# Kernel tuning notes

Measured on AMD Instinct MI355X. Metric: run time of the kernel, lower is better.

The kernel has to match this reference:

```python
import jax, jax.numpy as jnp
import numpy as np

DIM, HEADS, WIN = 256, 8, 8
HD = DIM // HEADS
SCALE = HD ** -0.5


def _rel_index(w):
    # Swin-style relative position index, computed statically in numpy
    coords = np.stack(np.meshgrid(np.arange(w), np.arange(w), indexing='ij'))  # (2,w,w)
    cf = coords.reshape(2, -1)                      # (2, w*w)
    rel = (cf[:, :, None] - cf[:, None, :]).transpose(1, 2, 0)  # (w*w, w*w, 2)
    rel = rel.copy()
    rel[:, :, 0] += w - 1
    rel[:, :, 1] += w - 1
    rel[:, :, 0] *= 2 * w - 1
    return rel.sum(-1)                              # (w*w, w*w)

REL_IDX = _rel_index(WIN)


def setup_inputs() -> dict:
    key = jax.random.key(0)
    ks = jax.random.split(key, 6)
    B, C, D, H, W = 8, DIM, 100, WIN, WIN
    return {
        'x': jax.random.normal(ks[0], (B, C, D, H, W), jnp.float32),
        'dwconv_w': jax.random.normal(ks[1], (C, C, 1, 3, 3), jnp.float32) * 0.02,
        'dwconv_b': jnp.zeros((C,), jnp.float32),
        'qkv_w': jax.random.normal(ks[2], (3 * C, C), jnp.float32) * 0.02,
        'qkv_b': jnp.zeros((3 * C,), jnp.float32),
        'proj_w': jax.random.normal(ks[3], (C, C), jnp.float32) * 0.02,
        'proj_b': jnp.zeros((C,), jnp.float32),
        'rpb_table': jax.random.normal(ks[4], ((2 * WIN - 1) ** 2, HEADS), jnp.float32) * 0.02,
    }


def reference(x, dwconv_w, dwconv_b, qkv_w, qkv_b, proj_w, proj_b, rpb_table):
    B, C, D, H, W = x.shape
    N = H * W
    # 'dwconv': full Conv3d, kernel (1,3,3), padding (0,1,1)
    xl = jax.lax.conv_general_dilated(
        x, dwconv_w, window_strides=(1, 1, 1),
        padding=[(0, 0), (1, 1), (1, 1)],
        dimension_numbers=('NCDHW', 'OIDHW', 'NCDHW'),
    ) + dwconv_b[None, :, None, None, None]
    # qkv: 1x1x1 conv == pointwise linear over channels
    qkv = jnp.einsum('oc,bcdhw->bodhw', qkv_w, xl) + qkv_b[None, :, None, None, None]
    # channel dim layout: (three, head, head_dim)
    qkv = qkv.reshape(B, 3, HEADS, HD, D, N)
    q, k, v = qkv[:, 0], qkv[:, 1], qkv[:, 2]      # each (B, HEADS, HD, D, N)
    attn = jnp.einsum('bhcdn,bhcdm->bdhnm', q * SCALE, k)  # (B, D, HEADS, N, N)
    bias = rpb_table[REL_IDX.reshape(-1)].reshape(N, N, HEADS).transpose(2, 0, 1)
    attn = jax.nn.softmax(attn + bias[None, None], axis=-1)
    xa = jnp.einsum('bdhnm,bhcdm->bhcdn', attn, v)  # (B, HEADS, HD, D, N)
    xa = xa.reshape(B, C, D, H, W)                  # channel = (head, head_dim)
    out = jnp.einsum('oc,bcdhw->bodhw', proj_w, xa) + proj_b[None, :, None, None, None]
    return out
```

## Files before the change

kernel.cpp:

```cpp
#include <hip/hip_runtime.h>
#include <cstdint>
#include <cstddef>

#define SCALEQ 0.17677669529663689f

typedef _Float16 half_t;
typedef _Float16 half8   __attribute__((ext_vector_type(8)));
typedef _Float16 half4v  __attribute__((ext_vector_type(4)));
typedef float    float4v __attribute__((ext_vector_type(4)));

#define WAIT_LDS()                                                            \
  do {                                                                        \
    asm volatile("s_waitcnt lgkmcnt(0)" ::: "memory");                        \
    __builtin_amdgcn_sched_barrier(0);                                        \
  } while (0)

__global__ __launch_bounds__(256) void prep_w(
    const float* __restrict__ dwconv_w, const float* __restrict__ qkv_w,
    const float* __restrict__ proj_w, const float* __restrict__ rpb,
    half_t* __restrict__ Wt, half_t* __restrict__ qw16,
    half_t* __restrict__ pw16, float* __restrict__ btab) {
  const int blk = blockIdx.x, t = threadIdx.x;
  if (blk < 144) {
    const int base = blk * 4096;
#pragma unroll
    for (int i = 0; i < 16; ++i) {
      int idx = base + i * 256 + t;
      int tap = idx >> 16;
      int og = (idx >> 12) & 15, kh = (idx >> 9) & 7;
      int l15o = (idx >> 5) & 15, c5 = idx & 31;
      int o = og * 16 + l15o, c = kh * 32 + c5;
      Wt[idx] = (half_t)dwconv_w[(o * 256 + c) * 9 + tap];
    }
  } else if (blk < 240) {
    const int base = (blk - 144) * 2048;
#pragma unroll
    for (int i = 0; i < 8; ++i) {
      int idx = base + i * 256 + t;
      float v = qkv_w[idx];
      if (idx < 65536) v *= SCALEQ;
      qw16[idx] = (half_t)v;
    }
  } else if (blk < 272) {
    const int base = (blk - 240) * 2048;
#pragma unroll
    for (int i = 0; i < 8; ++i) {
      int idx = base + i * 256 + t;
      pw16[idx] = (half_t)proj_w[idx];
    }
  } else {
    const int base = (blk - 272) * 2048;
#pragma unroll
    for (int i = 0; i < 8; ++i) {
      int idx = base + i * 256 + t;
      int hd = idx >> 12, n = (idx >> 6) & 63, m = idx & 63;
      int h1 = n >> 3, w1 = n & 7, h2 = m >> 3, w2 = m & 7;
      int ridx = (h1 - h2 + 7) * 15 + (w1 - w2 + 7);
      btab[idx] = rpb[ridx * 8 + hd];
    }
  }
}

__global__ __launch_bounds__(512)
__attribute__((amdgpu_waves_per_eu(4, 4))) void fused_all(
    const float* __restrict__ xg, const half_t* __restrict__ Wt,
    const float* __restrict__ convb, const half_t* __restrict__ qw,
    const float* __restrict__ qkvb, const float* __restrict__ btab,
    const half_t* __restrict__ pw, const float* __restrict__ projb,
    float* __restrict__ out32) {
  __shared__ __align__(16) half_t LS[36864];
  const int bd = blockIdx.x;
  const int tid = threadIdx.x;
  const int wave = tid >> 6, lane = tid & 63;
  const int l15 = lane & 15, quad = lane >> 4;
  const int head = wave;
  const int b = bd / 100, d = bd % 100;

  half_t* xlp = LS;
  half_t* xa = LS;
  float* T = (float*)LS;
  half_t* xpl = LS + 16384;
  half_t* buf = LS + 16384 + wave * 2560;
  float* tile = (float*)LS;

  const half_t* Wq0 = qw + head * 32 * 256;
  const half_t* Wk0 = qw + 65536 + head * 32 * 256;
  const half_t* Wv0 = qw + 131072 + head * 32 * 256;

  {
    const float* xb0 = xg + ((size_t)(b * 256) * 100 + d) * 64;
#pragma unroll
    for (int i = 0; i < 32; ++i) {
      const int c = i * 8 + wave;
      tile[c * 66 + lane] = xb0[(size_t)c * 6400 + lane];
    }
  }
  __syncthreads();

  half8 xr[4];
#pragma unroll
  for (int i = 0; i < 4; ++i) {
    const int c8 = wave * 4 + i;
#pragma unroll
    for (int j = 0; j < 8; ++j)
      xr[i][j] = (half_t)tile[(c8 * 8 + j) * 66 + lane];
  }
  __syncthreads();

  {
#pragma unroll
    for (int i = 0; i < 4; ++i) {
      const int c8 = wave * 4 + i;
      *(half8*)&xpl[lane * 256 + ((c8 ^ (lane & 7)) * 8)] = xr[i];
    }
    if (tid < 32) {
      half8 z = {};
      *(half8*)(xpl + 64 * 256 + tid * 8) = z;
    }
  }
  __syncthreads();

  {
    const int wwl = l15 & 7, hb = l15 >> 3;
    float4v acc[2][4];
#pragma unroll
    for (int mi = 0; mi < 2; ++mi)
#pragma unroll
      for (int ni = 0; ni < 4; ++ni) {
        float4v z = {0.f, 0.f, 0.f, 0.f};
        acc[mi][ni] = z;
      }
    const half_t* wv0 = Wt + (wave * 2) * 4096 + l15 * 32 + quad * 8;
#pragma unroll 1
    for (int tap = 0; tap < 9; ++tap) {
      const int th = tap / 3, tw = tap - th * 3;
      const half_t* wt = wv0 + tap * 65536;
      const int ww = wwl + tw;
      const int okw = (ww >= 1) & (ww <= 8);
      int rowv[4];
#pragma unroll
      for (int ni = 0; ni < 4; ++ni) {
        const int hh = hb + th + ni * 2;
        const int ok = okw & (hh >= 1) & (hh <= 8);
        rowv[ni] = ok ? ((hh - 1) * 8 + (ww - 1)) : 64;
      }
#pragma unroll
      for (int kh = 0; kh < 8; ++kh) {
        half8 af0 = *(const half8*)(wt + kh * 512);
        half8 af1 = *(const half8*)(wt + 4096 + kh * 512);
        half8 bf[4];
#pragma unroll
        for (int ni = 0; ni < 4; ++ni) {
          const int r = rowv[ni];
          bf[ni] = *(const half8*)&xpl[r * 256 + (((kh * 4 + quad) ^ (r & 7)) * 8)];
        }
#pragma unroll
        for (int ni = 0; ni < 4; ++ni) {
          acc[0][ni] = __builtin_amdgcn_mfma_f32_16x16x32_f16(af0, bf[ni], acc[0][ni], 0, 0, 0);
          acc[1][ni] = __builtin_amdgcn_mfma_f32_16x16x32_f16(af1, bf[ni], acc[1][ni], 0, 0, 0);
        }
      }
    }
#pragma unroll
    for (int mi = 0; mi < 2; ++mi) {
      const int o4 = wave * 32 + mi * 16 + quad * 4;
      const float4v b4 = *(const float4v*)&convb[o4];
      const int chunk = o4 >> 3;
      const int sub = (quad & 1) * 4;
#pragma unroll
      for (int ni = 0; ni < 4; ++ni) {
        const int px = ni * 16 + l15;
        half4v h;
        h.x = (half_t)(acc[mi][ni].x + b4.x);
        h.y = (half_t)(acc[mi][ni].y + b4.y);
        h.z = (half_t)(acc[mi][ni].z + b4.z);
        h.w = (half_t)(acc[mi][ni].w + b4.w);
        *(half4v*)&xlp[px * 256 + ((chunk ^ (px & 7)) * 8) + sub] = h;
      }
    }
  }

  __syncthreads();

  half8 aq[4];
  {
    float4v acc[2][4];
#pragma unroll
    for (int mi = 0; mi < 2; ++mi)
#pragma unroll
      for (int ni = 0; ni < 4; ++ni) {
        float4v z = {0.f, 0.f, 0.f, 0.f};
        acc[mi][ni] = z;
      }
#pragma unroll
    for (int kh = 0; kh < 8; ++kh) {
      half8 w0 = *(const half8*)(Wq0 + l15 * 256 + kh * 32 + quad * 8);
      half8 w1 = *(const half8*)(Wq0 + (16 + l15) * 256 + kh * 32 + quad * 8);
      half8 bf[4];
#pragma unroll
      for (int ni = 0; ni < 4; ++ni) {
        int r = ni * 16 + l15;
        bf[ni] = *(const half8*)&xlp[r * 256 + (((kh * 4 + quad) ^ (r & 7)) * 8)];
      }
#pragma unroll
      for (int ni = 0; ni < 4; ++ni) {
        acc[0][ni] = __builtin_amdgcn_mfma_f32_16x16x32_f16(w0, bf[ni], acc[0][ni], 0, 0, 0);
        acc[1][ni] = __builtin_amdgcn_mfma_f32_16x16x32_f16(w1, bf[ni], acc[1][ni], 0, 0, 0);
      }
    }
#pragma unroll
    for (int mi = 0; mi < 2; ++mi) {
      const float4v b4 = *(const float4v*)&qkvb[head * 32 + mi * 16 + quad * 4];
#pragma unroll
      for (int ni = 0; ni < 4; ++ni) {
        half4v h;
        h.x = (half_t)(acc[mi][ni].x + b4.x * SCALEQ);
        h.y = (half_t)(acc[mi][ni].y + b4.y * SCALEQ);
        h.z = (half_t)(acc[mi][ni].z + b4.z * SCALEQ);
        h.w = (half_t)(acc[mi][ni].w + b4.w * SCALEQ);
        *(half4v*)(buf + (ni * 16 + l15) * 40 + mi * 16 + quad * 4) = h;
      }
    }
    WAIT_LDS();
#pragma unroll
    for (int i = 0; i < 4; ++i)
      aq[i] = *(const half8*)(buf + (i * 16 + l15) * 40 + quad * 8);
    WAIT_LDS();
  }

  half8 bk[4];
  {
    float4v acc[2][4];
#pragma unroll
    for (int mi = 0; mi < 2; ++mi)
#pragma unroll
      for (int ni = 0; ni < 4; ++ni) {
        float4v z = {0.f, 0.f, 0.f, 0.f};
        acc[mi][ni] = z;
      }
#pragma unroll
    for (int kh = 0; kh < 8; ++kh) {
      half8 w0 = *(const half8*)(Wk0 + l15 * 256 + kh * 32 + quad * 8);
      half8 w1 = *(const half8*)(Wk0 + (16 + l15) * 256 + kh * 32 + quad * 8);
      half8 bf[4];
#pragma unroll
      for (int ni = 0; ni < 4; ++ni) {
        int r = ni * 16 + l15;
        bf[ni] = *(const half8*)&xlp[r * 256 + (((kh * 4 + quad) ^ (r & 7)) * 8)];
      }
#pragma unroll
      for (int ni = 0; ni < 4; ++ni) {
        acc[0][ni] = __builtin_amdgcn_mfma_f32_16x16x32_f16(w0, bf[ni], acc[0][ni], 0, 0, 0);
        acc[1][ni] = __builtin_amdgcn_mfma_f32_16x16x32_f16(w1, bf[ni], acc[1][ni], 0, 0, 0);
      }
    }
#pragma unroll
    for (int mi = 0; mi < 2; ++mi) {
      const float4v b4 = *(const float4v*)&qkvb[256 + head * 32 + mi * 16 + quad * 4];
#pragma unroll
      for (int ni = 0; ni < 4; ++ni) {
        half4v h;
        h.x = (half_t)(acc[mi][ni].x + b4.x);
        h.y = (half_t)(acc[mi][ni].y + b4.y);
        h.z = (half_t)(acc[mi][ni].z + b4.z);
        h.w = (half_t)(acc[mi][ni].w + b4.w);
        *(half4v*)(buf + (ni * 16 + l15) * 40 + mi * 16 + quad * 4) = h;
      }
    }
    WAIT_LDS();
#pragma unroll
    for (int i = 0; i < 4; ++i)
      bk[i] = *(const half8*)(buf + (i * 16 + l15) * 40 + quad * 8);
    WAIT_LDS();
  }

  {
    float4v acc[2][4];
#pragma unroll
    for (int mi = 0; mi < 2; ++mi)
#pragma unroll
      for (int ni = 0; ni < 4; ++ni) {
        float4v z = {0.f, 0.f, 0.f, 0.f};
        acc[mi][ni] = z;
      }
#pragma unroll
    for (int kh = 0; kh < 8; ++kh) {
      half8 w0 = *(const half8*)(Wv0 + l15 * 256 + kh * 32 + quad * 8);
      half8 w1 = *(const half8*)(Wv0 + (16 + l15) * 256 + kh * 32 + quad * 8);
      half8 bf[4];
#pragma unroll
      for (int ni = 0; ni < 4; ++ni) {
        int r = ni * 16 + l15;
        bf[ni] = *(const half8*)&xlp[r * 256 + (((kh * 4 + quad) ^ (r & 7)) * 8)];
      }
#pragma unroll
      for (int ni = 0; ni < 4; ++ni) {
        acc[0][ni] = __builtin_amdgcn_mfma_f32_16x16x32_f16(w0, bf[ni], acc[0][ni], 0, 0, 0);
        acc[1][ni] = __builtin_amdgcn_mfma_f32_16x16x32_f16(w1, bf[ni], acc[1][ni], 0, 0, 0);
      }
    }
#pragma unroll
    for (int mi = 0; mi < 2; ++mi) {
      const float4v b4 = *(const float4v*)&qkvb[512 + head * 32 + mi * 16 + quad * 4];
#pragma unroll
      for (int ni = 0; ni < 4; ++ni) {
#pragma unroll
        for (int iv = 0; iv < 4; ++iv)
          buf[(mi * 16 + quad * 4 + iv) * 72 + ni * 16 + l15] =
              (half_t)(acc[mi][ni][iv] + b4[iv]);
      }
    }
  }

  const float* bh = btab + head * 4096;
  float4v s[4][4];
#pragma unroll
  for (int ni = 0; ni < 4; ++ni)
#pragma unroll
    for (int mi = 0; mi < 4; ++mi) {
      float4v z = {0.f, 0.f, 0.f, 0.f};
      s[ni][mi] = __builtin_amdgcn_mfma_f32_16x16x32_f16(aq[ni], bk[mi], z, 0, 0, 0);
    }
#pragma unroll
  for (int ni = 0; ni < 4; ++ni)
#pragma unroll
    for (int i = 0; i < 4; ++i) {
      const int n = ni * 16 + quad * 4 + i;
#pragma unroll
      for (int mi = 0; mi < 4; ++mi)
        s[ni][mi][i] += bh[n * 64 + mi * 16 + l15];
    }
  float inv[4][4];
#pragma unroll
  for (int ni = 0; ni < 4; ++ni)
#pragma unroll
    for (int i = 0; i < 4; ++i) {
      float mx = fmaxf(fmaxf(s[ni][0][i], s[ni][1][i]), fmaxf(s[ni][2][i], s[ni][3][i]));
      for (int off = 1; off < 16; off <<= 1) mx = fmaxf(mx, __shfl_xor(mx, off));
      float sum = 0.f;
#pragma unroll
      for (int mi = 0; mi < 4; ++mi) {
        float e = __expf(s[ni][mi][i] - mx);
        s[ni][mi][i] = e;
        sum += e;
      }
      for (int off = 1; off < 16; off <<= 1) sum += __shfl_xor(sum, off);
      inv[ni][i] = 1.0f / sum;
    }
  half4v ph[4][4];
#pragma unroll
  for (int ni = 0; ni < 4; ++ni)
#pragma unroll
    for (int mi = 0; mi < 4; ++mi)
#pragma unroll
      for (int i = 0; i < 4; ++i)
        ph[ni][mi][i] = (half_t)(s[ni][mi][i] * inv[ni][i]);

  WAIT_LDS();
  half8 av[2][2];
#pragma unroll
  for (int ci = 0; ci < 2; ++ci)
#pragma unroll
    for (int k2 = 0; k2 < 2; ++k2)
      av[ci][k2] = *(const half8*)(buf + (ci * 16 + l15) * 72 + k2 * 32 + quad * 8);
  WAIT_LDS();

  float4v oa[2][4];
#pragma unroll
  for (int ci = 0; ci < 2; ++ci)
#pragma unroll
    for (int ni = 0; ni < 4; ++ni) {
      float4v z = {0.f, 0.f, 0.f, 0.f};
      oa[ci][ni] = z;
    }
#pragma unroll
  for (int k2 = 0; k2 < 2; ++k2) {
#pragma unroll
    for (int mi2 = 0; mi2 < 2; ++mi2) {
      const int mi = k2 * 2 + mi2;
#pragma unroll
      for (int ni = 0; ni < 4; ++ni)
#pragma unroll
        for (int i = 0; i < 4; ++i) {
          const int n = ni * 16 + quad * 4 + i;
          buf[n * 40 + mi2 * 16 + l15] = ph[ni][mi][i];
        }
    }
    WAIT_LDS();
    half8 bp[4];
#pragma unroll
    for (int ni = 0; ni < 4; ++ni)
      bp[ni] = *(const half8*)(buf + (ni * 16 + l15) * 40 + quad * 8);
    WAIT_LDS();
#pragma unroll
    for (int ni = 0; ni < 4; ++ni)
#pragma unroll
      for (int ci = 0; ci < 2; ++ci)
        oa[ci][ni] = __builtin_amdgcn_mfma_f32_16x16x32_f16(av[ci][k2], bp[ni], oa[ci][ni], 0, 0, 0);
  }

  __syncthreads();

#pragma unroll
  for (int ci = 0; ci < 2; ++ci)
#pragma unroll
    for (int ni = 0; ni < 4; ++ni) {
      half4v h = {(half_t)oa[ci][ni].x, (half_t)oa[ci][ni].y,
                  (half_t)oa[ci][ni].z, (half_t)oa[ci][ni].w};
      *(half4v*)(xa + (ni * 16 + l15) * 264 + head * 32 + ci * 16 + quad * 4) = h;
    }
  __syncthreads();

  const half_t* Wp0 = pw + wave * 32 * 256;
  float4v pacc[2][4];
#pragma unroll
  for (int mi = 0; mi < 2; ++mi)
#pragma unroll
    for (int ni = 0; ni < 4; ++ni) {
      float4v z = {0.f, 0.f, 0.f, 0.f};
      pacc[mi][ni] = z;
    }
#pragma unroll
  for (int kh = 0; kh < 8; ++kh) {
    half8 w0 = *(const half8*)(Wp0 + l15 * 256 + kh * 32 + quad * 8);
    half8 w1 = *(const half8*)(Wp0 + (16 + l15) * 256 + kh * 32 + quad * 8);
    half8 bf[4];
#pragma unroll
    for (int ni = 0; ni < 4; ++ni)
      bf[ni] = *(const half8*)&xa[(ni * 16 + l15) * 264 + kh * 32 + quad * 8];
#pragma unroll
    for (int ni = 0; ni < 4; ++ni) {
      pacc[0][ni] = __builtin_amdgcn_mfma_f32_16x16x32_f16(w0, bf[ni], pacc[0][ni], 0, 0, 0);
      pacc[1][ni] = __builtin_amdgcn_mfma_f32_16x16x32_f16(w1, bf[ni], pacc[1][ni], 0, 0, 0);
    }
  }
#pragma unroll
  for (int mi = 0; mi < 2; ++mi) {
    const float4v b4 = *(const float4v*)&projb[wave * 32 + mi * 16 + quad * 4];
#pragma unroll
    for (int ni = 0; ni < 4; ++ni) {
      pacc[mi][ni].x += b4.x;
      pacc[mi][ni].y += b4.y;
      pacc[mi][ni].z += b4.z;
      pacc[mi][ni].w += b4.w;
    }
  }

  const size_t bdbase = (size_t)b * 1638400 + (size_t)d * 64;
  const int tr = tid >> 3;
  const int col0 = (tid & 7) * 4;
  for (int r = 0; r < 4; ++r) {
    __syncthreads();
    if ((wave >> 1) == r) {
      const int rb = (wave & 1) * 32;
#pragma unroll
      for (int mi = 0; mi < 2; ++mi)
#pragma unroll
        for (int ni = 0; ni < 4; ++ni)
#pragma unroll
          for (int iv = 0; iv < 4; ++iv)
            T[(rb + mi * 16 + quad * 4 + iv) * 68 + ni * 16 + l15] = pacc[mi][ni][iv];
    }
    __syncthreads();
    const int o = r * 64 + tr;
    float* dst = out32 + bdbase + (size_t)o * 6400 + col0;
    const float* srcT = &T[tr * 68 + col0];
    float4v v0 = *(const float4v*)srcT;
    float4v v1 = *(const float4v*)(srcT + 32);
    __builtin_nontemporal_store(v0, (float4v*)dst);
    __builtin_nontemporal_store(v1, (float4v*)(dst + 32));
  }
}

extern "C" void kernel_launch(void* const* d_in, const int* in_sizes, int n_in,
                              void* d_out, int out_size, void* d_ws, size_t ws_size,
                              hipStream_t stream) {
  const float* x        = (const float*)d_in[0];
  const float* dwconv_w = (const float*)d_in[1];
  const float* dwconv_b = (const float*)d_in[2];
  const float* qkv_w    = (const float*)d_in[3];
  const float* qkv_b    = (const float*)d_in[4];
  const float* proj_w   = (const float*)d_in[5];
  const float* proj_b   = (const float*)d_in[6];
  const float* rpb      = (const float*)d_in[7];
  float* out = (float*)d_out;

  char* ws = (char*)d_ws;
  size_t off = 0;
  half_t* Wt   = (half_t*)(ws + off); off += 1179648;
  half_t* qw16 = (half_t*)(ws + off); off += 393216;
  half_t* pw16 = (half_t*)(ws + off); off += 131072;
  float*  btab = (float*)(ws + off);  off += 131072;

  prep_w<<<288, 256, 0, stream>>>(dwconv_w, qkv_w, proj_w, rpb,
                                  Wt, qw16, pw16, btab);
  fused_all<<<800, 512, 0, stream>>>(x, Wt, dwconv_b, qw16, qkv_b, btab,
                                     pw16, proj_b, out);
}
```

Measured before the change: 265.6 us.

## Shrink shared memory footprint to fit more blocks per CU

```diff
diff --git a/kernel.cpp b/kernel.cpp
--- a/kernel.cpp
+++ b/kernel.cpp
@@ -62,13 +62,13 @@
 }
 
 __global__ __launch_bounds__(512)
-__attribute__((amdgpu_waves_per_eu(4, 4))) void fused_all(
+__attribute__((amdgpu_waves_per_eu(4))) void fused_all(
     const float* __restrict__ xg, const half_t* __restrict__ Wt,
     const float* __restrict__ convb, const half_t* __restrict__ qw,
     const float* __restrict__ qkvb, const float* __restrict__ btab,
     const half_t* __restrict__ pw, const float* __restrict__ projb,
     float* __restrict__ out32) {
-  __shared__ __align__(16) half_t LS[36864];
+  __shared__ __align__(16) half_t LS[26880];
   const int bd = blockIdx.x;
   const int tid = threadIdx.x;
   const int wave = tid >> 6, lane = tid & 63;
@@ -76,43 +76,43 @@
   const int head = wave;
   const int b = bd / 100, d = bd % 100;
 
+  half_t* xpl = LS;
   half_t* xlp = LS;
   half_t* xa = LS;
   float* T = (float*)LS;
-  half_t* xpl = LS + 16384;
-  half_t* buf = LS + 16384 + wave * 2560;
   float* tile = (float*)LS;
+  half_t* buf = LS + 16640 + wave * 1280;
 
   const half_t* Wq0 = qw + head * 32 * 256;
   const half_t* Wk0 = qw + 65536 + head * 32 * 256;
   const half_t* Wv0 = qw + 131072 + head * 32 * 256;
 
+  half8 xr[4];
   {
     const float* xb0 = xg + ((size_t)(b * 256) * 100 + d) * 64;
-#pragma unroll
-    for (int i = 0; i < 32; ++i) {
-      const int c = i * 8 + wave;
-      tile[c * 66 + lane] = xb0[(size_t)c * 6400 + lane];
-    }
-  }
-  __syncthreads();
-
-  half8 xr[4];
-#pragma unroll
-  for (int i = 0; i < 4; ++i) {
-    const int c8 = wave * 4 + i;
-#pragma unroll
-    for (int j = 0; j < 8; ++j)
-      xr[i][j] = (half_t)tile[(c8 * 8 + j) * 66 + lane];
-  }
-  __syncthreads();
-
-  {
-#pragma unroll
-    for (int i = 0; i < 4; ++i) {
-      const int c8 = wave * 4 + i;
-      *(half8*)&xpl[lane * 256 + ((c8 ^ (lane & 7)) * 8)] = xr[i];
-    }
+    for (int hf = 0; hf < 2; ++hf) {
+#pragma unroll
+      for (int i = 0; i < 16; ++i) {
+        const int cl = i * 8 + wave;
+        tile[cl * 65 + lane] = xb0[(size_t)(hf * 128 + cl) * 6400 + lane];
+      }
+      __syncthreads();
+#pragma unroll
+      for (int ii = 0; ii < 2; ++ii) {
+        const int c8l = wave * 2 + ii;
+#pragma unroll
+        for (int j = 0; j < 8; ++j)
+          xr[hf * 2 + ii][j] = (half_t)tile[(c8l * 8 + j) * 65 + lane];
+      }
+      __syncthreads();
+    }
+#pragma unroll
+    for (int hf = 0; hf < 2; ++hf)
+#pragma unroll
+      for (int ii = 0; ii < 2; ++ii) {
+        const int c8 = hf * 16 + wave * 2 + ii;
+        *(half8*)&xpl[lane * 256 + ((c8 ^ (lane & 7)) * 8)] = xr[hf * 2 + ii];
+      }
     if (tid < 32) {
       half8 z = {};
       *(half8*)(xpl + 64 * 256 + tid * 8) = z;
@@ -161,6 +161,7 @@
         }
       }
     }
+    __syncthreads();
 #pragma unroll
     for (int mi = 0; mi < 2; ++mi) {
       const int o4 = wave * 32 + mi * 16 + quad * 4;
@@ -209,23 +210,27 @@
       }
     }
 #pragma unroll
-    for (int mi = 0; mi < 2; ++mi) {
-      const float4v b4 = *(const float4v*)&qkvb[head * 32 + mi * 16 + quad * 4];
-#pragma unroll
-      for (int ni = 0; ni < 4; ++ni) {
-        half4v h;
-        h.x = (half_t)(acc[mi][ni].x + b4.x * SCALEQ);
-        h.y = (half_t)(acc[mi][ni].y + b4.y * SCALEQ);
-        h.z = (half_t)(acc[mi][ni].z + b4.z * SCALEQ);
-        h.w = (half_t)(acc[mi][ni].w + b4.w * SCALEQ);
-        *(half4v*)(buf + (ni * 16 + l15) * 40 + mi * 16 + quad * 4) = h;
-      }
-    }
-    WAIT_LDS();
-#pragma unroll
-    for (int i = 0; i < 4; ++i)
-      aq[i] = *(const half8*)(buf + (i * 16 + l15) * 40 + quad * 8);
-    WAIT_LDS();
+    for (int h2 = 0; h2 < 2; ++h2) {
+#pragma unroll
+      for (int mi = 0; mi < 2; ++mi) {
+        const float4v b4 = *(const float4v*)&qkvb[head * 32 + mi * 16 + quad * 4];
+#pragma unroll
+        for (int nj = 0; nj < 2; ++nj) {
+          const int ni = h2 * 2 + nj;
+          half4v h;
+          h.x = (half_t)(acc[mi][ni].x + b4.x * SCALEQ);
+          h.y = (half_t)(acc[mi][ni].y + b4.y * SCALEQ);
+          h.z = (half_t)(acc[mi][ni].z + b4.z * SCALEQ);
+          h.w = (half_t)(acc[mi][ni].w + b4.w * SCALEQ);
+          *(half4v*)(buf + (nj * 16 + l15) * 40 + mi * 16 + quad * 4) = h;
+        }
+      }
+      WAIT_LDS();
+#pragma unroll
+      for (int j = 0; j < 2; ++j)
+        aq[h2 * 2 + j] = *(const half8*)(buf + (j * 16 + l15) * 40 + quad * 8);
+      WAIT_LDS();
+    }
   }
 
   half8 bk[4];
@@ -255,25 +260,30 @@
       }
     }
 #pragma unroll
-    for (int mi = 0; mi < 2; ++mi) {
-      const float4v b4 = *(const float4v*)&qkvb[256 + head * 32 + mi * 16 + quad * 4];
-#pragma unroll
-      for (int ni = 0; ni < 4; ++ni) {
-        half4v h;
-        h.x = (half_t)(acc[mi][ni].x + b4.x);
-        h.y = (half_t)(acc[mi][ni].y + b4.y);
-        h.z = (half_t)(acc[mi][ni].z + b4.z);
-        h.w = (half_t)(acc[mi][ni].w + b4.w);
-        *(half4v*)(buf + (ni * 16 + l15) * 40 + mi * 16 + quad * 4) = h;
-      }
-    }
-    WAIT_LDS();
-#pragma unroll
-    for (int i = 0; i < 4; ++i)
-      bk[i] = *(const half8*)(buf + (i * 16 + l15) * 40 + quad * 8);
-    WAIT_LDS();
-  }
-
+    for (int h2 = 0; h2 < 2; ++h2) {
+#pragma unroll
+      for (int mi = 0; mi < 2; ++mi) {
+        const float4v b4 = *(const float4v*)&qkvb[256 + head * 32 + mi * 16 + quad * 4];
+#pragma unroll
+        for (int nj = 0; nj < 2; ++nj) {
+          const int ni = h2 * 2 + nj;
+          half4v h;
+          h.x = (half_t)(acc[mi][ni].x + b4.x);
+          h.y = (half_t)(acc[mi][ni].y + b4.y);
+          h.z = (half_t)(acc[mi][ni].z + b4.z);
+          h.w = (half_t)(acc[mi][ni].w + b4.w);
+          *(half4v*)(buf + (nj * 16 + l15) * 40 + mi * 16 + quad * 4) = h;
+        }
+      }
+      WAIT_LDS();
+#pragma unroll
+      for (int j = 0; j < 2; ++j)
+        bk[h2 * 2 + j] = *(const half8*)(buf + (j * 16 + l15) * 40 + quad * 8);
+      WAIT_LDS();
+    }
+  }
+
+  half8 av[2][2];
   {
     float4v acc[2][4];
 #pragma unroll
@@ -303,12 +313,16 @@
     for (int mi = 0; mi < 2; ++mi) {
       const float4v b4 = *(const float4v*)&qkvb[512 + head * 32 + mi * 16 + quad * 4];
 #pragma unroll
-      for (int ni = 0; ni < 4; ++ni) {
+      for (int ni = 0; ni < 4; ++ni)
 #pragma unroll
         for (int iv = 0; iv < 4; ++iv)
-          buf[(mi * 16 + quad * 4 + iv) * 72 + ni * 16 + l15] =
+          buf[(quad * 4 + iv) * 72 + ni * 16 + l15] =
               (half_t)(acc[mi][ni][iv] + b4[iv]);
-      }
+      WAIT_LDS();
+#pragma unroll
+      for (int k2 = 0; k2 < 2; ++k2)
+        av[mi][k2] = *(const half8*)(buf + l15 * 72 + k2 * 32 + quad * 8);
+      WAIT_LDS();
     }
   }
 
@@ -356,15 +370,6 @@
       for (int i = 0; i < 4; ++i)
         ph[ni][mi][i] = (half_t)(s[ni][mi][i] * inv[ni][i]);
 
-  WAIT_LDS();
-  half8 av[2][2];
-#pragma unroll
-  for (int ci = 0; ci < 2; ++ci)
-#pragma unroll
-    for (int k2 = 0; k2 < 2; ++k2)
-      av[ci][k2] = *(const half8*)(buf + (ci * 16 + l15) * 72 + k2 * 32 + quad * 8);
-  WAIT_LDS();
-
   float4v oa[2][4];
 #pragma unroll
   for (int ci = 0; ci < 2; ++ci)
@@ -376,27 +381,31 @@
 #pragma unroll
   for (int k2 = 0; k2 < 2; ++k2) {
 #pragma unroll
-    for (int mi2 = 0; mi2 < 2; ++mi2) {
-      const int mi = k2 * 2 + mi2;
-#pragma unroll
-      for (int ni = 0; ni < 4; ++ni)
-#pragma unroll
-        for (int i = 0; i < 4; ++i) {
-          const int n = ni * 16 + quad * 4 + i;
-          buf[n * 40 + mi2 * 16 + l15] = ph[ni][mi][i];
+    for (int rh = 0; rh < 2; ++rh) {
+#pragma unroll
+      for (int nj = 0; nj < 2; ++nj) {
+        const int ni = rh * 2 + nj;
+#pragma unroll
+        for (int mi2 = 0; mi2 < 2; ++mi2) {
+          const int mi = k2 * 2 + mi2;
+#pragma unroll
+          for (int i = 0; i < 4; ++i)
+            buf[(nj * 16 + quad * 4 + i) * 36 + mi2 * 16 + l15] = ph[ni][mi][i];
         }
-    }
-    WAIT_LDS();
-    half8 bp[4];
-#pragma unroll
-    for (int ni = 0; ni < 4; ++ni)
-      bp[ni] = *(const half8*)(buf + (ni * 16 + l15) * 40 + quad * 8);
-    WAIT_LDS();
-#pragma unroll
-    for (int ni = 0; ni < 4; ++ni)
-#pragma unroll
-      for (int ci = 0; ci < 2; ++ci)
-        oa[ci][ni] = __builtin_amdgcn_mfma_f32_16x16x32_f16(av[ci][k2], bp[ni], oa[ci][ni], 0, 0, 0);
+      }
+      WAIT_LDS();
+      half8 bpn[2];
+#pragma unroll
+      for (int nj = 0; nj < 2; ++nj)
+        bpn[nj] = *(const half8*)(buf + (nj * 16 + l15) * 36 + quad * 8);
+      WAIT_LDS();
+#pragma unroll
+      for (int nj = 0; nj < 2; ++nj)
+#pragma unroll
+        for (int ci = 0; ci < 2; ++ci)
+          oa[ci][rh * 2 + nj] = __builtin_amdgcn_mfma_f32_16x16x32_f16(
+              av[ci][k2], bpn[nj], oa[ci][rh * 2 + nj], 0, 0, 0);
+    }
   }
 
   __syncthreads();
```

After: 255.6 us. 3.8% less time.
